# Performance work log

Hardware: AMD Instinct MI355X
Metric: run time of the kernel (lower is better)

## Reference

```python
import jax, jax.numpy as jnp
import numpy as np

B, S, V, E, H, L = 32, 256, 10000, 512, 1024, 3
SCALE = 1.0
RESCALE = 12 // L  # rescale_rate


def setup_inputs() -> dict:
    key = jax.random.key(0)
    ks = jax.random.split(key, 12)
    s = 0.02
    return {
        "src": jax.random.randint(ks[0], (B, S), 0, V),
        "fix_pred": jax.random.normal(ks[1], (B, S), jnp.float32),
        "emb": jax.random.normal(ks[2], (V, E), jnp.float32) * s,
        "W_lin": jax.random.normal(ks[3], (H, E), jnp.float32) * s,
        "b_lin": jnp.zeros((H,), jnp.float32),
        "W_ih": jax.random.normal(ks[4], (L, 4 * H, H), jnp.float32) * s,
        "W_hh": jax.random.normal(ks[5], (L, 4 * H, H), jnp.float32) * s,
        "b_ih": jnp.zeros((L, 4 * H), jnp.float32),
        "b_hh": jnp.zeros((L, 4 * H), jnp.float32),
        "fc_W1": jax.random.normal(ks[6], (E, H), jnp.float32) * s,
        "fc_b1": jnp.zeros((E,), jnp.float32),
        "fc_W2": jax.random.normal(ks[7], (V, E), jnp.float32) * s,
        "fc_b2": jnp.zeros((V,), jnp.float32),
        "h0": jnp.zeros((L, B, H), jnp.float32),
        "c0": jnp.zeros((L, B, H), jnp.float32),
    }


def reference(src, fix_pred, emb, W_lin, b_lin, W_ih, W_hh, b_ih, b_hh,
              fc_W1, fc_b1, fc_W2, fc_b2, h0, c0):
    # fix_predict with use_norm: layer_norm over seq dim, rescale to ~[0, 12]
    mu = jnp.mean(fix_pred, axis=1, keepdims=True)
    var = jnp.var(fix_pred, axis=1, keepdims=True)
    fp = (fix_pred - mu) * jax.lax.rsqrt(var + 1e-5)
    fp = (fp + 1.96) / 3.92 * 12.0                      # [B, S]

    # embedding + input projection (dropout rates are 0 -> identity)
    input_x = jnp.einsum('bse,he->sbh', emb[src], W_lin) + b_lin  # [S, B, H]

    alpha0 = (11.0 - fp.T)[..., None] / RESCALE         # [S, B, 1]
    x = jnp.zeros_like(input_x)
    for l in range(L):
        alpha = alpha0 - l
        mask = jax.nn.sigmoid(alpha * SCALE)            # [S, B, 1]
        gate = jax.nn.sigmoid((alpha + 1.0) * SCALE) - mask
        inp_seq = x * (1.0 - gate) + input_x * gate     # [S, B, H]
        Wi, Wh, bi, bh = W_ih[l], W_hh[l], b_ih[l], b_hh[l]

        def step(carry, xs):
            h, c = carry
            inp, m = xs
            g = inp @ Wi.T + bi + h @ Wh.T + bh         # [B, 4H]
            gi, gf, gg, go = jnp.split(g, 4, axis=-1)   # torch gate order i,f,g,o
            c_new = jax.nn.sigmoid(gf) * c + jax.nn.sigmoid(gi) * jnp.tanh(gg)
            h_new = jax.nn.sigmoid(go) * jnp.tanh(c_new)
            c_new = c_new * (1.0 - m) + c * m           # adaptive skip/copy blend
            h_new = h_new * (1.0 - m) + h * m
            return (h_new, c_new), h_new

        _, x = jax.lax.scan(step, (h0[l], c0[l]), (inp_seq, mask))

    out = jnp.transpose(x, (1, 0, 2))                   # [B, S, H]
    hid = jnp.tanh(out @ fc_W1.T + fc_b1)               # [B, S, E]
    return hid @ fc_W2.T + fc_b2                        # [B, S, V]
```

## Files before the change

kernel.cpp:

```cpp
#include <hip/hip_runtime.h>
#include <math.h>

#define Bb 32
#define Ss 256
#define Vv 10000
#define Ee 512
#define Hh 1024
#define Ll 3
#define FH 4096

typedef short short8 __attribute__((ext_vector_type(8)));
typedef float floatx4 __attribute__((ext_vector_type(4)));

__device__ __forceinline__ float sigf(float x) { return 1.0f / (1.0f + expf(-x)); }

__device__ __forceinline__ unsigned pack_hl(float x) {
    unsigned u = __float_as_uint(x);
    unsigned r = u + 0x7fff + ((u >> 16) & 1);
    unsigned hi = r >> 16;
    float hf = __uint_as_float(hi << 16);
    float l = x - hf;
    unsigned ul = __float_as_uint(l);
    unsigned rl = ul + 0x7fff + ((ul >> 16) & 1);
    return hi | ((rl >> 16) << 16);
}
__device__ __forceinline__ void split_hl(float x, unsigned short& h, unsigned short& l) {
    unsigned p = pack_hl(x);
    h = (unsigned short)(p & 0xffff);
    l = (unsigned short)(p >> 16);
}

__global__ __launch_bounds__(256) void pack_split(
    const float* __restrict__ src, unsigned* __restrict__ dst, int n4)
{
    int i = blockIdx.x * 256 + threadIdx.x;
    if (i < n4) {
        float4 v = ((const float4*)src)[i];
        uint4 o;
        o.x = pack_hl(v.x); o.y = pack_hl(v.y); o.z = pack_hl(v.z); o.w = pack_hl(v.w);
        ((uint4*)dst)[i] = o;
    }
}

__global__ __launch_bounds__(256) void maskgate_kernel(
    const float* __restrict__ fp_in, float* __restrict__ mask, float* __restrict__ gate)
{
    __shared__ float red[256];
    int b = blockIdx.x, t = threadIdx.x;
    float v = fp_in[b * Ss + t];
    red[t] = v;
    __syncthreads();
    for (int o = 128; o > 0; o >>= 1) { if (t < o) red[t] += red[t + o]; __syncthreads(); }
    float mu = red[0] * (1.0f / Ss);
    __syncthreads();
    float d = v - mu;
    red[t] = d * d;
    __syncthreads();
    for (int o = 128; o > 0; o >>= 1) { if (t < o) red[t] += red[t + o]; __syncthreads(); }
    float var = red[0] * (1.0f / Ss);
    float fp = d * (1.0f / sqrtf(var + 1e-5f));
    fp = (fp + 1.96f) / 3.92f * 12.0f;
    float alpha0 = (11.0f - fp) * 0.25f;
    for (int l = 0; l < Ll; ++l) {
        float a = alpha0 - (float)l;
        float m = sigf(a);
        float g = sigf(a + 1.0f) - m;
        mask[l * (Ss * Bb) + t * Bb + b] = m;
        gate[l * (Ss * Bb) + t * Bb + b] = g;
    }
}

template <int MODE>
__global__ __launch_bounds__(256) void gemm_nt(
    const float* __restrict__ Amat, const float* __restrict__ Bmat,
    const float* __restrict__ bias1,
    float* __restrict__ Cmat, int M, int N, int K,
    const int* __restrict__ srcIdx, const float* __restrict__ embTab)
{
    __shared__ float As[16][68];
    __shared__ float Bs[16][68];
    int t = threadIdx.x;
    int tx = t & 15, ty = t >> 4;
    int n0 = blockIdx.x * 64, m0 = blockIdx.y * 64;
    int li = t >> 2;
    int lk = (t & 3) * 4;
    float acc[4][4];
#pragma unroll
    for (int y = 0; y < 4; ++y)
#pragma unroll
        for (int x = 0; x < 4; ++x) acc[y][x] = 0.0f;

    for (int k0 = 0; k0 < K; k0 += 16) {
        float a0, a1, a2, a3;
        {
            int r = m0 + li;
            if (MODE == 0) {
                int idx = srcIdx[(r & 31) * Ss + (r >> 5)];
                float4 v = *(const float4*)(embTab + (size_t)idx * K + (k0 + lk));
                a0 = v.x; a1 = v.y; a2 = v.z; a3 = v.w;
            } else {
                float4 v = *(const float4*)(Amat + (size_t)r * K + (k0 + lk));
                a0 = v.x; a1 = v.y; a2 = v.z; a3 = v.w;
            }
        }
        As[lk + 0][li] = a0; As[lk + 1][li] = a1; As[lk + 2][li] = a2; As[lk + 3][li] = a3;
        {
            int n = n0 + li;
            float b0 = 0.f, b1 = 0.f, b2 = 0.f, b3 = 0.f;
            if (n < N) {
                float4 v = *(const float4*)(Bmat + (size_t)n * K + (k0 + lk));
                b0 = v.x; b1 = v.y; b2 = v.z; b3 = v.w;
            }
            Bs[lk + 0][li] = b0; Bs[lk + 1][li] = b1; Bs[lk + 2][li] = b2; Bs[lk + 3][li] = b3;
        }
        __syncthreads();
#pragma unroll
        for (int kk = 0; kk < 16; ++kk) {
            float4 av = *(const float4*)&As[kk][ty * 4];
            float4 bv = *(const float4*)&Bs[kk][tx * 4];
            float avc[4] = {av.x, av.y, av.z, av.w};
            float bvc[4] = {bv.x, bv.y, bv.z, bv.w};
#pragma unroll
            for (int y = 0; y < 4; ++y)
#pragma unroll
                for (int x = 0; x < 4; ++x)
                    acc[y][x] = fmaf(avc[y], bvc[x], acc[y][x]);
        }
        __syncthreads();
    }
#pragma unroll
    for (int y = 0; y < 4; ++y) {
        int r = m0 + ty * 4 + y;
#pragma unroll
        for (int x = 0; x < 4; ++x) {
            int n = n0 + tx * 4 + x;
            if (n < N) {
                float vv = acc[y][x];
                if (MODE == 0) Cmat[(size_t)r * N + n] = vv + bias1[n];
                else           Cmat[(size_t)r * N + n] = tanhf(vv + bias1[n]);
            }
        }
    }
}

template <int MODE>
__global__ __launch_bounds__(256) void gemm_mfma(
    const float* __restrict__ Amat, const unsigned* __restrict__ Bp,
    const float* __restrict__ bias1, const float* __restrict__ bias2,
    float* __restrict__ Cmat, int M, int N, int K,
    const float* __restrict__ xb, const float* __restrict__ ixb,
    const float* __restrict__ gateArr, int rowOff,
    float* __restrict__ outDst)
{
    __shared__ unsigned short As_h[128][40];
    __shared__ unsigned short As_l[128][40];
    __shared__ unsigned short Bs_h[128][40];
    __shared__ unsigned short Bs_l[128][40];

    const int t = threadIdx.x;
    const int n0 = blockIdx.x * 128, m0 = blockIdx.y * 128;
    const int lane = t & 63, w = t >> 6;
    const int mb = (w & 1) * 64, nb = (w >> 1) * 64;
    const int row = lane & 15, grp8 = (lane >> 4) * 8;

    const int arow = t >> 1;
    const int kseg = (t & 1) * 16;

    float gblend = 0.0f;
    const float* aptr = nullptr;
    const float* xptr = nullptr;
    if (MODE == 1 || MODE == 2) {
        int rg = rowOff + m0 + arow;
        gblend = gateArr[rg];
        aptr = ixb + (size_t)rg * K;
        if (MODE == 2) xptr = xb + (size_t)rg * K;
    } else {
        aptr = Amat + (size_t)(m0 + arow) * K;
    }
    const int bn = n0 + arow;
    const unsigned* bptr = Bp + (size_t)(bn < N ? bn : 0) * K;
    const bool bvalid = (bn < N);

    floatx4 acc[4][4];
#pragma unroll
    for (int i = 0; i < 4; ++i)
#pragma unroll
        for (int j = 0; j < 4; ++j)
            acc[i][j] = (floatx4){0.f, 0.f, 0.f, 0.f};

    for (int k0 = 0; k0 < K; k0 += 32) {
        unsigned short hbuf[16], lbuf[16];
#pragma unroll
        for (int u = 0; u < 4; ++u) {
            float4 vi = *(const float4*)(aptr + k0 + kseg + u * 4);
            float vals[4] = {vi.x, vi.y, vi.z, vi.w};
            if (MODE == 1) {
#pragma unroll
                for (int c = 0; c < 4; ++c) vals[c] *= gblend;
            } else if (MODE == 2) {
                float4 vx = *(const float4*)(xptr + k0 + kseg + u * 4);
                float xs[4] = {vx.x, vx.y, vx.z, vx.w};
#pragma unroll
                for (int c = 0; c < 4; ++c) vals[c] = xs[c] + (vals[c] - xs[c]) * gblend;
            }
#pragma unroll
            for (int c = 0; c < 4; ++c) split_hl(vals[c], hbuf[u * 4 + c], lbuf[u * 4 + c]);
        }
        {
            uint4 ph, pl;
            ph.x = hbuf[0] | ((unsigned)hbuf[1] << 16);
            ph.y = hbuf[2] | ((unsigned)hbuf[3] << 16);
            ph.z = hbuf[4] | ((unsigned)hbuf[5] << 16);
            ph.w = hbuf[6] | ((unsigned)hbuf[7] << 16);
            pl.x = lbuf[0] | ((unsigned)lbuf[1] << 16);
            pl.y = lbuf[2] | ((unsigned)lbuf[3] << 16);
            pl.z = lbuf[4] | ((unsigned)lbuf[5] << 16);
            pl.w = lbuf[6] | ((unsigned)lbuf[7] << 16);
            *(uint4*)&As_h[arow][kseg] = ph;
            *(uint4*)&As_l[arow][kseg] = pl;
            uint4 ph2, pl2;
            ph2.x = hbuf[8] | ((unsigned)hbuf[9] << 16);
            ph2.y = hbuf[10] | ((unsigned)hbuf[11] << 16);
            ph2.z = hbuf[12] | ((unsigned)hbuf[13] << 16);
            ph2.w = hbuf[14] | ((unsigned)hbuf[15] << 16);
            pl2.x = lbuf[8] | ((unsigned)lbuf[9] << 16);
            pl2.y = lbuf[10] | ((unsigned)lbuf[11] << 16);
            pl2.z = lbuf[12] | ((unsigned)lbuf[13] << 16);
            pl2.w = lbuf[14] | ((unsigned)lbuf[15] << 16);
            *(uint4*)&As_h[arow][kseg + 8] = ph2;
            *(uint4*)&As_l[arow][kseg + 8] = pl2;
        }
        {
            unsigned short bh[16], bl[16];
            if (bvalid) {
#pragma unroll
                for (int u = 0; u < 4; ++u) {
                    uint4 q = *(const uint4*)(bptr + k0 + kseg + u * 4);
                    unsigned qs[4] = {q.x, q.y, q.z, q.w};
#pragma unroll
                    for (int c = 0; c < 4; ++c) {
                        bh[u * 4 + c] = (unsigned short)(qs[c] & 0xffff);
                        bl[u * 4 + c] = (unsigned short)(qs[c] >> 16);
                    }
                }
            } else {
#pragma unroll
                for (int c = 0; c < 16; ++c) { bh[c] = 0; bl[c] = 0; }
            }
            uint4 ph, pl;
            ph.x = bh[0] | ((unsigned)bh[1] << 16);
            ph.y = bh[2] | ((unsigned)bh[3] << 16);
            ph.z = bh[4] | ((unsigned)bh[5] << 16);
            ph.w = bh[6] | ((unsigned)bh[7] << 16);
            pl.x = bl[0] | ((unsigned)bl[1] << 16);
            pl.y = bl[2] | ((unsigned)bl[3] << 16);
            pl.z = bl[4] | ((unsigned)bl[5] << 16);
            pl.w = bl[6] | ((unsigned)bl[7] << 16);
            *(uint4*)&Bs_h[arow][kseg] = ph;
            *(uint4*)&Bs_l[arow][kseg] = pl;
            uint4 ph2, pl2;
            ph2.x = bh[8] | ((unsigned)bh[9] << 16);
            ph2.y = bh[10] | ((unsigned)bh[11] << 16);
            ph2.z = bh[12] | ((unsigned)bh[13] << 16);
            ph2.w = bh[14] | ((unsigned)bh[15] << 16);
            pl2.x = bl[8] | ((unsigned)bl[9] << 16);
            pl2.y = bl[10] | ((unsigned)bl[11] << 16);
            pl2.z = bl[12] | ((unsigned)bl[13] << 16);
            pl2.w = bl[14] | ((unsigned)bl[15] << 16);
            *(uint4*)&Bs_h[arow][kseg + 8] = ph2;
            *(uint4*)&Bs_l[arow][kseg + 8] = pl2;
        }
        __syncthreads();
        short8 ah[4], al[4], bh8[4], bl8[4];
#pragma unroll
        for (int i = 0; i < 4; ++i) {
            ah[i] = *(const short8*)&As_h[mb + i * 16 + row][grp8];
            al[i] = *(const short8*)&As_l[mb + i * 16 + row][grp8];
            bh8[i] = *(const short8*)&Bs_h[nb + i * 16 + row][grp8];
            bl8[i] = *(const short8*)&Bs_l[nb + i * 16 + row][grp8];
        }
#pragma unroll
        for (int i = 0; i < 4; ++i)
#pragma unroll
            for (int j = 0; j < 4; ++j) {
                acc[i][j] = __builtin_amdgcn_mfma_f32_16x16x32_bf16(ah[i], bh8[j], acc[i][j], 0, 0, 0);
                acc[i][j] = __builtin_amdgcn_mfma_f32_16x16x32_bf16(al[i], bh8[j], acc[i][j], 0, 0, 0);
                acc[i][j] = __builtin_amdgcn_mfma_f32_16x16x32_bf16(ah[i], bl8[j], acc[i][j], 0, 0, 0);
            }
        __syncthreads();
    }

    const int grp = lane >> 4;
#pragma unroll
    for (int i = 0; i < 4; ++i) {
        int mbase = m0 + mb + i * 16 + grp * 4;
#pragma unroll
        for (int j = 0; j < 4; ++j) {
            int n = n0 + nb + j * 16 + (lane & 15);
#pragma unroll
            for (int r = 0; r < 4; ++r) {
                float vv = acc[i][j][r];
                int mm = mbase + r;
                if (MODE == 4) {
                    if (n < N)
                        outDst[((size_t)(mm & 31) * Ss + (mm >> 5)) * Vv + n] = vv + bias1[n];
                } else {
                    Cmat[(size_t)mm * N + n] = vv + bias1[n] + bias2[n];
                }
            }
        }
    }
}

__global__ __launch_bounds__(256) void lstm_step(
    const float* __restrict__ Gp,
    const float* __restrict__ Wh,
    const float* __restrict__ maskp,
    const float* __restrict__ hprev,
    float* __restrict__ hnext,
    float* __restrict__ cbuf,
    float* __restrict__ xout)
{
    __shared__ float hs[32 * 132];
    __shared__ float gbuf[16 * 32];
    int t = threadIdx.x;
    int b = t & 31, rr = t >> 5;
    int q = rr >> 1, dd = rr & 1;
    int j0 = blockIdx.x * 4;
    int row0 = q * Hh + j0 + dd;
    int row1 = row0 + 2;
    const float* w0 = Wh + (size_t)row0 * Hh;
    const float* w1 = Wh + (size_t)row1 * Hh;
    float acc0 = 0.0f, acc1 = 0.0f;

    for (int kc = 0; kc < Hh; kc += 128) {
#pragma unroll
        for (int i = 0; i < 4; ++i) {
            int f4 = i * 256 + t;
            int bl = f4 >> 5, k4 = f4 & 31;
            float4 v = *(const float4*)(hprev + bl * Hh + kc + k4 * 4);
            *(float4*)(hs + bl * 132 + k4 * 4) = v;
        }
        __syncthreads();
        const float* hb = hs + b * 132;
#pragma unroll
        for (int k4 = 0; k4 < 32; ++k4) {
            float4 hv = *(const float4*)(hb + k4 * 4);
            float4 wa = *(const float4*)(w0 + kc + k4 * 4);
            float4 wc = *(const float4*)(w1 + kc + k4 * 4);
            acc0 = fmaf(wa.x, hv.x, acc0); acc0 = fmaf(wa.y, hv.y, acc0);
            acc0 = fmaf(wa.z, hv.z, acc0); acc0 = fmaf(wa.w, hv.w, acc0);
            acc1 = fmaf(wc.x, hv.x, acc1); acc1 = fmaf(wc.y, hv.y, acc1);
            acc1 = fmaf(wc.z, hv.z, acc1); acc1 = fmaf(wc.w, hv.w, acc1);
        }
        __syncthreads();
    }
    acc0 += Gp[(size_t)b * FH + row0];
    acc1 += Gp[(size_t)b * FH + row1];
    gbuf[(q * 4 + dd) * 32 + b] = acc0;
    gbuf[(q * 4 + dd + 2) * 32 + b] = acc1;
    __syncthreads();
    if (t < 128) {
        int b2 = t & 31, d2 = t >> 5;
        int j = j0 + d2;
        float gi = gbuf[(0 * 4 + d2) * 32 + b2];
        float gf = gbuf[(1 * 4 + d2) * 32 + b2];
        float gg = gbuf[(2 * 4 + d2) * 32 + b2];
        float go = gbuf[(3 * 4 + d2) * 32 + b2];
        float m  = maskp[b2];
        float c_old = cbuf[b2 * Hh + j];
        float h_old = hprev[b2 * Hh + j];
        float ct = sigf(gf) * c_old + sigf(gi) * tanhf(gg);
        float ht = sigf(go) * tanhf(ct);
        float cn = ct + (c_old - ct) * m;
        float hn = ht + (h_old - ht) * m;
        cbuf[b2 * Hh + j] = cn;
        hnext[b2 * Hh + j] = hn;
        xout[b2 * Hh + j] = hn;
    }
}

__global__ __launch_bounds__(256) void init_hc(
    const float* __restrict__ h0, const float* __restrict__ c0,
    float* __restrict__ hb0, float* __restrict__ cb)
{
    int i = blockIdx.x * 256 + threadIdx.x;
    hb0[i] = h0[i];
    cb[i] = c0[i];
}

extern "C" void kernel_launch(void* const* d_in, const int* in_sizes, int n_in,
                              void* d_out, int out_size, void* d_ws, size_t ws_size,
                              hipStream_t stream)
{
    const int*   src      = (const int*)  d_in[0];
    const float* fix_pred = (const float*)d_in[1];
    const float* emb      = (const float*)d_in[2];
    const float* W_lin    = (const float*)d_in[3];
    const float* b_lin    = (const float*)d_in[4];
    const float* W_ih     = (const float*)d_in[5];
    const float* W_hh     = (const float*)d_in[6];
    const float* b_ih     = (const float*)d_in[7];
    const float* b_hh     = (const float*)d_in[8];
    const float* fc_W1    = (const float*)d_in[9];
    const float* fc_b1    = (const float*)d_in[10];
    const float* fc_W2    = (const float*)d_in[11];
    const float* fc_b2    = (const float*)d_in[12];
    const float* h0       = (const float*)d_in[13];
    const float* c0       = (const float*)d_in[14];
    float* out = (float*)d_out;

    float* ws    = (float*)d_ws;
    float* ix    = ws;
    float* xbuf  = ix + 8388608;
    float* Gch   = xbuf + 8388608;
    float* hid   = Gch;
    unsigned* wpack = (unsigned*)(Gch + 8388608);
    float* hb    = (float*)(wpack + 4194304);
    float* cb    = hb + 65536;
    float* mask  = cb + 32768;
    float* gate  = mask + 24576;

    maskgate_kernel<<<32, 256, 0, stream>>>(fix_pred, mask, gate);

    gemm_nt<0><<<dim3(16, 128), 256, 0, stream>>>(
        nullptr, W_lin, b_lin, ix, 8192, 1024, 512, src, emb);

    for (int l = 0; l < Ll; ++l) {
        pack_split<<<4096, 256, 0, stream>>>(W_ih + (size_t)l * FH * Hh, wpack, 1048576);
        init_hc<<<128, 256, 0, stream>>>(h0 + (size_t)l * 32768, c0 + (size_t)l * 32768, hb, cb);
        const float* Wh = W_hh + (size_t)l * FH * Hh;
        const float* bi = b_ih + (size_t)l * FH;
        const float* bh = b_hh + (size_t)l * FH;
        for (int ch = 0; ch < 4; ++ch) {
            int rowOff = ch * 2048;
            if (l == 0) {
                gemm_mfma<1><<<dim3(32, 16), 256, 0, stream>>>(
                    nullptr, wpack, bi, bh, Gch, 2048, 4096, 1024,
                    nullptr, ix, gate + l * 8192, rowOff, nullptr);
            } else {
                gemm_mfma<2><<<dim3(32, 16), 256, 0, stream>>>(
                    nullptr, wpack, bi, bh, Gch, 2048, 4096, 1024,
                    xbuf, ix, gate + l * 8192, rowOff, nullptr);
            }
            for (int sl = 0; sl < 64; ++sl) {
                int s = ch * 64 + sl;
                lstm_step<<<256, 256, 0, stream>>>(
                    Gch + (size_t)sl * 32 * FH,
                    Wh,
                    mask + l * 8192 + s * 32,
                    hb + (s & 1) * 32768,
                    hb + ((s + 1) & 1) * 32768,
                    cb,
                    xbuf + (size_t)s * 32768);
            }
        }
    }

    gemm_nt<3><<<dim3(8, 128), 256, 0, stream>>>(
        xbuf, fc_W1, fc_b1, hid, 8192, 512, 1024, nullptr, nullptr);

    unsigned* w2pack = (unsigned*)ix;
    pack_split<<<5000, 256, 0, stream>>>(fc_W2, w2pack, 1280000);
    gemm_mfma<4><<<dim3(79, 64), 256, 0, stream>>>(
        hid, w2pack, fc_b2, nullptr, nullptr, 8192, 10000, 512,
        nullptr, nullptr, nullptr, 0, out);
}
```

Before: 26.16 ms.

## Replace per-timestep LSTM launches with persistent cooperative kernel using grid sync

Swaps the 64 per-timestep lstm_step launches per chunk for one cooperative kernel that loops over the timesteps and uses grid.sync between them. Cell and hidden state for each block's columns stay in registers, and the mask is staged in shared memory. The K reduction is now split across 8 thread groups with a shared-memory combine, so 512 threads cover 16 gate rows. This removes launch overhead and state reloads, at the cost of relying on grid-wide barrier latency and on all 256 blocks being co-resident.

```diff
diff --git a/kernel.cpp b/kernel.cpp
--- a/kernel.cpp
+++ b/kernel.cpp
@@ -1,5 +1,8 @@
 #include <hip/hip_runtime.h>
+#include <hip/hip_cooperative_groups.h>
 #include <math.h>
+
+namespace cg = cooperative_groups;
 
 #define Bb 32
 #define Ss 256
@@ -312,72 +315,107 @@
     }
 }
 
-__global__ __launch_bounds__(256) void lstm_step(
-    const float* __restrict__ Gp,
+__global__ __launch_bounds__(512) void lstm_chunk(
+    const float* __restrict__ Gc,
     const float* __restrict__ Wh,
-    const float* __restrict__ maskp,
-    const float* __restrict__ hprev,
-    float* __restrict__ hnext,
-    float* __restrict__ cbuf,
-    float* __restrict__ xout)
+    const float* __restrict__ maskL,
+    float* __restrict__ hb,
+    float* __restrict__ cb,
+    float* __restrict__ xout,
+    int s0)
 {
     __shared__ float hs[32 * 132];
-    __shared__ float gbuf[16 * 32];
-    int t = threadIdx.x;
-    int b = t & 31, rr = t >> 5;
-    int q = rr >> 1, dd = rr & 1;
-    int j0 = blockIdx.x * 4;
-    int row0 = q * Hh + j0 + dd;
-    int row1 = row0 + 2;
-    const float* w0 = Wh + (size_t)row0 * Hh;
-    const float* w1 = Wh + (size_t)row1 * Hh;
-    float acc0 = 0.0f, acc1 = 0.0f;
-
-    for (int kc = 0; kc < Hh; kc += 128) {
-#pragma unroll
-        for (int i = 0; i < 4; ++i) {
-            int f4 = i * 256 + t;
-            int bl = f4 >> 5, k4 = f4 & 31;
-            float4 v = *(const float4*)(hprev + bl * Hh + kc + k4 * 4);
-            *(float4*)(hs + bl * 132 + k4 * 4) = v;
+    __shared__ float gbuf[8 * 16 * 32];
+    __shared__ float msk[64 * 32];
+
+    cg::grid_group grid = cg::this_grid();
+
+    const int t  = threadIdx.x;
+    const int j0 = blockIdx.x * 4;
+    const int b  = t & 31;
+    const int rg = (t >> 5) & 1;
+    const int kh = t >> 6;
+
+    for (int i = t; i < 64 * 32; i += 512) msk[i] = maskL[s0 * 32 + i];
+
+    const int b2 = t & 31, d2 = (t >> 5) & 3;
+    float c_reg = 0.f, h_reg = 0.f;
+    if (t < 128) {
+        c_reg = cb[b2 * Hh + j0 + d2];
+        h_reg = hb[b2 * Hh + j0 + d2];
+    }
+
+    const float* wr[8];
+#pragma unroll
+    for (int ri = 0; ri < 8; ++ri) {
+        int lr = rg * 8 + ri;
+        wr[ri] = Wh + (size_t)((lr >> 2) * Hh + j0 + (lr & 3)) * Hh + kh * 16;
+    }
+
+    for (int s = 0; s < 64; ++s) {
+        const float* hprev = hb + ((s0 + s) & 1) * 32768;
+        float* hnext       = hb + ((s0 + s + 1) & 1) * 32768;
+
+        float ax[8], ay[8], az[8], aw[8];
+#pragma unroll
+        for (int ri = 0; ri < 8; ++ri) { ax[ri] = ay[ri] = az[ri] = aw[ri] = 0.f; }
+
+        for (int kc = 0; kc < Hh; kc += 128) {
+            {
+                int i0 = t;
+                int bl = i0 >> 5, k4 = i0 & 31;
+                *(float4*)(hs + bl * 132 + k4 * 4) =
+                    *(const float4*)(hprev + bl * Hh + kc + k4 * 4);
+                int i1 = t + 512;
+                bl = i1 >> 5; k4 = i1 & 31;
+                *(float4*)(hs + bl * 132 + k4 * 4) =
+                    *(const float4*)(hprev + bl * Hh + kc + k4 * 4);
+            }
+            __syncthreads();
+            const float* hp = hs + b * 132 + kh * 16;
+#pragma unroll
+            for (int u = 0; u < 4; ++u) {
+                float4 hv = *(const float4*)(hp + u * 4);
+#pragma unroll
+                for (int ri = 0; ri < 8; ++ri) {
+                    float4 wv = *(const float4*)(wr[ri] + kc + u * 4);
+                    ax[ri] = fmaf(wv.x, hv.x, ax[ri]);
+                    ay[ri] = fmaf(wv.y, hv.y, ay[ri]);
+                    az[ri] = fmaf(wv.z, hv.z, az[ri]);
+                    aw[ri] = fmaf(wv.w, hv.w, aw[ri]);
+                }
+            }
+            __syncthreads();
+        }
+#pragma unroll
+        for (int ri = 0; ri < 8; ++ri) {
+            int lr = rg * 8 + ri;
+            gbuf[kh * 512 + lr * 32 + b] = (ax[ri] + ay[ri]) + (az[ri] + aw[ri]);
         }
         __syncthreads();
-        const float* hb = hs + b * 132;
-#pragma unroll
-        for (int k4 = 0; k4 < 32; ++k4) {
-            float4 hv = *(const float4*)(hb + k4 * 4);
-            float4 wa = *(const float4*)(w0 + kc + k4 * 4);
-            float4 wc = *(const float4*)(w1 + kc + k4 * 4);
-            acc0 = fmaf(wa.x, hv.x, acc0); acc0 = fmaf(wa.y, hv.y, acc0);
-            acc0 = fmaf(wa.z, hv.z, acc0); acc0 = fmaf(wa.w, hv.w, acc0);
-            acc1 = fmaf(wc.x, hv.x, acc1); acc1 = fmaf(wc.y, hv.y, acc1);
-            acc1 = fmaf(wc.z, hv.z, acc1); acc1 = fmaf(wc.w, hv.w, acc1);
-        }
-        __syncthreads();
-    }
-    acc0 += Gp[(size_t)b * FH + row0];
-    acc1 += Gp[(size_t)b * FH + row1];
-    gbuf[(q * 4 + dd) * 32 + b] = acc0;
-    gbuf[(q * 4 + dd + 2) * 32 + b] = acc1;
-    __syncthreads();
-    if (t < 128) {
-        int b2 = t & 31, d2 = t >> 5;
-        int j = j0 + d2;
-        float gi = gbuf[(0 * 4 + d2) * 32 + b2];
-        float gf = gbuf[(1 * 4 + d2) * 32 + b2];
-        float gg = gbuf[(2 * 4 + d2) * 32 + b2];
-        float go = gbuf[(3 * 4 + d2) * 32 + b2];
-        float m  = maskp[b2];
-        float c_old = cbuf[b2 * Hh + j];
-        float h_old = hprev[b2 * Hh + j];
-        float ct = sigf(gf) * c_old + sigf(gi) * tanhf(gg);
-        float ht = sigf(go) * tanhf(ct);
-        float cn = ct + (c_old - ct) * m;
-        float hn = ht + (h_old - ht) * m;
-        cbuf[b2 * Hh + j] = cn;
-        hnext[b2 * Hh + j] = hn;
-        xout[b2 * Hh + j] = hn;
-    }
+        if (t < 128) {
+            float g4[4];
+#pragma unroll
+            for (int q = 0; q < 4; ++q) {
+                int lr = q * 4 + d2;
+                float sum = Gc[(size_t)s * (32 * FH) + b2 * FH + q * Hh + j0 + d2];
+#pragma unroll
+                for (int k2 = 0; k2 < 8; ++k2) sum += gbuf[k2 * 512 + lr * 32 + b2];
+                g4[q] = sum;
+            }
+            float m  = msk[s * 32 + b2];
+            float ct = sigf(g4[1]) * c_reg + sigf(g4[0]) * tanhf(g4[2]);
+            float ht = sigf(g4[3]) * tanhf(ct);
+            c_reg = ct + (c_reg - ct) * m;
+            h_reg = ht + (h_reg - ht) * m;
+            int j = j0 + d2;
+            hnext[b2 * Hh + j] = h_reg;
+            xout[(size_t)(s0 + s) * 32768 + b2 * Hh + j] = h_reg;
+            __threadfence();
+        }
+        grid.sync();
+    }
+    if (t < 128) cb[b2 * Hh + j0 + d2] = c_reg;
 }
 
 __global__ __launch_bounds__(256) void init_hc(
@@ -443,16 +481,20 @@
                     nullptr, wpack, bi, bh, Gch, 2048, 4096, 1024,
                     xbuf, ix, gate + l * 8192, rowOff, nullptr);
             }
-            for (int sl = 0; sl < 64; ++sl) {
-                int s = ch * 64 + sl;
-                lstm_step<<<256, 256, 0, stream>>>(
-                    Gch + (size_t)sl * 32 * FH,
-                    Wh,
-                    mask + l * 8192 + s * 32,
-                    hb + (s & 1) * 32768,
-                    hb + ((s + 1) & 1) * 32768,
-                    cb,
-                    xbuf + (size_t)s * 32768);
+            {
+                const float* GcArg   = Gch;
+                const float* WhArg   = Wh;
+                const float* maskArg = mask + l * 8192;
+                float* hbArg = hb;
+                float* cbArg = cb;
+                float* xoArg = xbuf;
+                int s0 = ch * 64;
+                void* args[] = {
+                    (void*)&GcArg, (void*)&WhArg, (void*)&maskArg,
+                    (void*)&hbArg, (void*)&cbArg, (void*)&xoArg, (void*)&s0
+                };
+                hipLaunchCooperativeKernel((const void*)lstm_chunk,
+                                           dim3(256), dim3(512), args, 0, stream);
             }
         }
     }
```

Measured after the change: 58.45 ms. 123% more time.
